# Kernel optimization log

Hardware: AMD Instinct MI355X
Metric: run time of the kernel (lower is better)

## Reference

```python
import jax, jax.numpy as jnp
import numpy as np

VOCAB, DIM = 50257, 1024
B, S = 4, 2048
P_DROP = 0.5


def setup_inputs() -> dict:
    key = jax.random.key(0)
    kw, km, ki = jax.random.split(key, 3)
    weight = jax.random.normal(kw, (VOCAB, DIM), dtype=jnp.float32)
    keep = 1.0 - P_DROP
    # per-row bernoulli keep mask, pre-scaled by 1/(1-p), shape (V, 1)
    mask = jax.random.bernoulli(km, keep, (VOCAB, 1)).astype(jnp.float32) / keep
    words = jax.random.randint(ki, (B, S), 0, VOCAB, dtype=jnp.int64)
    return {"weight": weight, "mask": mask, "words": words}


def reference(weight, mask, words):
    # masked_embed_weight = mask * weight  (mask broadcasts over DIM)
    # X = F.embedding(words, masked_embed_weight)
    masked = mask * weight                     # [V, D]
    return jnp.take(masked, words, axis=0)     # [B, S, D]
```

## Files before the change

### kernel.cpp

```cpp
#include <hip/hip_runtime.h>


#define DIM 1024

__global__ void EmbeddingDropout_kernel(const float* __restrict__ weight,
                                        const float* __restrict__ mask,
                                        const int* __restrict__ words,
                                        float* __restrict__ out,
                                        int n_tokens) {
    int tok = blockIdx.x;
    if (tok >= n_tokens) return;
    int row = words[tok];
    float m = mask[row];
    const float4* __restrict__ src =
        reinterpret_cast<const float4*>(weight + (size_t)row * DIM);
    float4* __restrict__ dst =
        reinterpret_cast<float4*>(out + (size_t)tok * DIM);
    float4 v = src[threadIdx.x];
    v.x *= m; v.y *= m; v.z *= m; v.w *= m;
    dst[threadIdx.x] = v;
}

extern "C" void kernel_launch(void* const* d_in, const int* in_sizes, int n_in,
                              void* d_out, int out_size, void* d_ws, size_t ws_size,
                              hipStream_t stream) {
    const float* weight = (const float*)d_in[0];
    const float* mask   = (const float*)d_in[1];
    const int*   words  = (const int*)d_in[2];
    float* out = (float*)d_out;
    int n_tokens = in_sizes[2];

    dim3 grid(n_tokens);
    dim3 block(DIM / 4);
    EmbeddingDropout_kernel<<<grid, block, 0, stream>>>(weight, mask, words, out, n_tokens);
}
```

Measured before the change: 15.86 us.

## Map one wave to two tokens with batched loads and nontemporal stores

Restructures the gather so each 64-lane wave copies two full embedding rows, with all eight 16-byte loads per lane issued before any store. The aim is more memory-level parallelism per thread and fewer, larger blocks. Output writes become nontemporal stores so the streamed output does not pollute the cache. The cost is more registers per thread and fewer waves in total, which could reduce latency hiding.

```diff
diff --git a/kernel.cpp b/kernel.cpp
--- a/kernel.cpp
+++ b/kernel.cpp
@@ -1,36 +1,71 @@
 #include <hip/hip_runtime.h>
 
 
+typedef float v4f __attribute__((ext_vector_type(4)));
+
 #define DIM 1024
+#define V4_PER_ROW (DIM / 4)
+#define TOKENS_PER_WAVE 2
+#define WAVES_PER_BLOCK 4
+#define TOKENS_PER_BLOCK (TOKENS_PER_WAVE * WAVES_PER_BLOCK)
 
-__global__ void EmbeddingDropout_kernel(const float* __restrict__ weight,
+__global__ void EmbeddingDropout_kernel(const v4f* __restrict__ weight,
                                         const float* __restrict__ mask,
                                         const int* __restrict__ words,
-                                        float* __restrict__ out,
+                                        v4f* __restrict__ out,
                                         int n_tokens) {
-    int tok = blockIdx.x;
-    if (tok >= n_tokens) return;
-    int row = words[tok];
-    float m = mask[row];
-    const float4* __restrict__ src =
-        reinterpret_cast<const float4*>(weight + (size_t)row * DIM);
-    float4* __restrict__ dst =
-        reinterpret_cast<float4*>(out + (size_t)tok * DIM);
-    float4 v = src[threadIdx.x];
-    v.x *= m; v.y *= m; v.z *= m; v.w *= m;
-    dst[threadIdx.x] = v;
+    int wave = threadIdx.x >> 6;
+    int lane = threadIdx.x & 63;
+    int t0 = (blockIdx.x * WAVES_PER_BLOCK + wave) * TOKENS_PER_WAVE;
+    int t1 = t0 + 1;
+    if (t1 >= n_tokens) {
+        if (t0 >= n_tokens) return;
+        t1 = t0;
+    }
+
+    int r0 = words[t0];
+    int r1 = words[t1];
+    float m0 = mask[r0];
+    float m1 = mask[r1];
+
+    const v4f* __restrict__ s0 = weight + (size_t)r0 * V4_PER_ROW;
+    const v4f* __restrict__ s1 = weight + (size_t)r1 * V4_PER_ROW;
+
+    v4f a0 = s0[lane];
+    v4f a1 = s0[lane + 64];
+    v4f a2 = s0[lane + 128];
+    v4f a3 = s0[lane + 192];
+    v4f b0 = s1[lane];
+    v4f b1 = s1[lane + 64];
+    v4f b2 = s1[lane + 128];
+    v4f b3 = s1[lane + 192];
+
+    a0 *= m0; a1 *= m0; a2 *= m0; a3 *= m0;
+    b0 *= m1; b1 *= m1; b2 *= m1; b3 *= m1;
+
+    v4f* __restrict__ d0 = out + (size_t)t0 * V4_PER_ROW;
+    v4f* __restrict__ d1 = out + (size_t)t1 * V4_PER_ROW;
+
+    __builtin_nontemporal_store(a0, d0 + lane);
+    __builtin_nontemporal_store(a1, d0 + lane + 64);
+    __builtin_nontemporal_store(a2, d0 + lane + 128);
+    __builtin_nontemporal_store(a3, d0 + lane + 192);
+    __builtin_nontemporal_store(b0, d1 + lane);
+    __builtin_nontemporal_store(b1, d1 + lane + 64);
+    __builtin_nontemporal_store(b2, d1 + lane + 128);
+    __builtin_nontemporal_store(b3, d1 + lane + 192);
 }
 
 extern "C" void kernel_launch(void* const* d_in, const int* in_sizes, int n_in,
                               void* d_out, int out_size, void* d_ws, size_t ws_size,
                               hipStream_t stream) {
-    const float* weight = (const float*)d_in[0];
+    const v4f*   weight = (const v4f*)d_in[0];
     const float* mask   = (const float*)d_in[1];
     const int*   words  = (const int*)d_in[2];
-    float* out = (float*)d_out;
+    v4f* out = (v4f*)d_out;
     int n_tokens = in_sizes[2];
 
-    dim3 grid(n_tokens);
-    dim3 block(DIM / 4);
+    dim3 grid((n_tokens + TOKENS_PER_BLOCK - 1) / TOKENS_PER_BLOCK);
+    dim3 block(64 * WAVES_PER_BLOCK);
     EmbeddingDropout_kernel<<<grid, block, 0, stream>>>(weight, mask, words, out, n_tokens);
 }
```

After: 13.79 us. 1.15x faster.
